# Kernel tuning notes

Hardware: AMD Instinct MI355X
Metric: run time of the kernel (lower is better)

Reference implementation:

```python
import jax, jax.numpy as jnp
import numpy as np

BN_EPS = 1e-5
NUM_HEADS = 16


def setup_inputs() -> dict:
    key = jax.random.key(0)
    k1, k2 = jax.random.split(key)
    B, F, E = 8, 1024, 1024
    x = jax.random.normal(k1, (B, F, E), dtype=jnp.float32)
    # xavier_uniform for Linear(E, 3E): bound = sqrt(6/(E + 3E))
    bound = float(np.sqrt(6.0 / (E + 3 * E)))
    W_qkv = jax.random.uniform(k2, (3 * E, E), minval=-bound, maxval=bound, dtype=jnp.float32)
    b_qkv = jnp.zeros((3 * E,), dtype=jnp.float32)
    gamma = jnp.ones((F,), dtype=jnp.float32)
    beta = jnp.zeros((F,), dtype=jnp.float32)
    return {"x": x, "gamma": gamma, "beta": beta, "W_qkv": W_qkv, "b_qkv": b_qkv}


def reference(x, gamma, beta, W_qkv, b_qkv):
    B, F, E = x.shape
    H = NUM_HEADS
    hd = E // H
    # BatchNorm1d(features_dim) in training mode: channels = F axis,
    # stats over (batch, embed) dims, biased variance.
    mean = jnp.mean(x, axis=(0, 2), keepdims=True)          # [1,F,1]
    var = jnp.mean((x - mean) ** 2, axis=(0, 2), keepdims=True)
    xn = (x - mean) * jax.lax.rsqrt(var + BN_EPS)
    xn = xn * gamma[None, :, None] + beta[None, :, None]
    # QKV projection: torch Linear -> xn @ W^T + b
    qkv = jnp.einsum('bfe,oe->bfo', xn, W_qkv) + b_qkv       # [B,F,3E]
    qkv = qkv.reshape(B, F, H, 3 * hd).transpose(0, 2, 1, 3) # [B,H,F,3hd]
    q, k, v = jnp.split(qkv, 3, axis=-1)                     # each [B,H,F,hd]
    scale = 1.0 / jnp.sqrt(jnp.float32(hd))
    logits = jnp.einsum('bhqd,bhkd->bhqk', q, k) * scale     # [B,H,F,F]
    attn = jax.nn.softmax(logits, axis=-1)
    values = jnp.einsum('bhqk,bhkd->bhqd', attn, v)          # [B,H,F,hd]
    values = values.transpose(0, 2, 1, 3).reshape(B, F, E)
    return values
```

## Files before the change

### kernel.cpp

```cpp
#include <hip/hip_runtime.h>

typedef unsigned short u16;
typedef unsigned int   u32;

typedef __bf16 bf16x8 __attribute__((ext_vector_type(8)));
typedef float  f32x4  __attribute__((ext_vector_type(4)));

typedef const __attribute__((address_space(1))) void* gas_ptr;
typedef __attribute__((address_space(3))) void* las_ptr;

__device__ __forceinline__ u16 f2bf(float f) {
  u32 u = __builtin_bit_cast(u32, f);
  u += 0x7fffu + ((u >> 16) & 1u);
  return (u16)(u >> 16);
}
__device__ __forceinline__ float bf2f(u16 u) {
  return __builtin_bit_cast(float, ((u32)u) << 16);
}
__device__ __forceinline__ u32 cvtpk(float a, float b) {
  u32 r;
  asm("v_cvt_pk_bf16_f32 %0, %1, %2" : "=v"(r) : "v"(a), "v"(b));
  return r;
}
__device__ __forceinline__ float fexp2(float x) {
  return __builtin_amdgcn_exp2f(x);
}

__global__ __launch_bounds__(256) void bn_norm_kernel(
    const float* __restrict__ x, const float* __restrict__ gamma,
    const float* __restrict__ beta, u16* __restrict__ xn) {
  const int F = 1024, E = 1024;
  int f = blockIdx.x;
  __shared__ float sh[8192];
  __shared__ float ps[4], pq[4], sc[2];

  const float* xf = x + (size_t)f * E;
  float ls = 0.f, lq = 0.f;
  for (int i = threadIdx.x; i < 8192; i += 256) {
    int b = i >> 10, e = i & 1023;
    float v = xf[(size_t)b * F * E + e];
    sh[i] = v;
    ls += v;
    lq += v * v;
  }
  #pragma unroll
  for (int o = 32; o > 0; o >>= 1) {
    ls += __shfl_down(ls, o, 64);
    lq += __shfl_down(lq, o, 64);
  }
  int w = threadIdx.x >> 6;
  if ((threadIdx.x & 63) == 0) { ps[w] = ls; pq[w] = lq; }
  __syncthreads();
  if (threadIdx.x == 0) {
    float s = ps[0] + ps[1] + ps[2] + ps[3];
    float q = pq[0] + pq[1] + pq[2] + pq[3];
    float mean = s * (1.f / 8192.f);
    float var = q * (1.f / 8192.f) - mean * mean;
    float scale = gamma[f] * rsqrtf(var + 1e-5f);
    sc[0] = scale;
    sc[1] = beta[f] - mean * scale;
  }
  __syncthreads();
  float scale = sc[0], shift = sc[1];
  for (int i = threadIdx.x; i < 8192; i += 256) {
    int b = i >> 10, e = i & 1023;
    xn[((size_t)(b * F + f)) * E + e] = f2bf(sh[i] * scale + shift);
  }
}

__global__ __launch_bounds__(256) void wconv_kernel(
    const float* __restrict__ W, u16* __restrict__ Wb) {
  const int total = 3072 * 1024 / 4;
  for (int i = blockIdx.x * 256 + threadIdx.x; i < total; i += gridDim.x * 256) {
    float4 v = ((const float4*)W)[i];
    ushort4 o;
    o.x = f2bf(v.x); o.y = f2bf(v.y); o.z = f2bf(v.z); o.w = f2bf(v.w);
    ((ushort4*)Wb)[i] = o;
  }
}

__global__ __launch_bounds__(512) void gemm_qkv_kernel(
    const u16* __restrict__ A, const u16* __restrict__ Bw,
    const float* __restrict__ bias, u16* __restrict__ C) {
  const int K = 1024, N = 3072;
  __shared__ u16 LA[2 * 16384];
  __shared__ u16 LB[2 * 16384];

  int bid = blockIdx.x;
  int m0 = (bid & 31) * 256, n0 = (bid >> 5) * 256;

  int tid = threadIdx.x;
  int lane = tid & 63, w = tid >> 6;
  int wm = w >> 2, wn = w & 3;
  int q = lane & 15, g = lane >> 4;
  int qs7 = q & 7;

  int srow8 = tid >> 3;
  int sc = tid & 7;

  f32x4 acc[8][4] = {};

  #define STAGE_A(buf, t)                                                    \
    do {                                                                     \
      _Pragma("unroll")                                                      \
      for (int j2 = 0; j2 < 4; ++j2) {                                       \
        int row = j2 * 64 + srow8;                                           \
        const u16* src = A + (size_t)(m0 + row) * K + (t) * 64               \
                           + ((sc ^ (row & 7)) * 8);                         \
        __builtin_amdgcn_global_load_lds((gas_ptr)src,                       \
            (las_ptr)&LA[(buf) * 16384 + row * 64 + sc * 8], 16, 0, 0);      \
      }                                                                      \
    } while (0)
  #define STAGE_B(buf, t)                                                    \
    do {                                                                     \
      _Pragma("unroll")                                                      \
      for (int j2 = 0; j2 < 4; ++j2) {                                       \
        int row = j2 * 64 + srow8;                                           \
        const u16* src = Bw + (size_t)(n0 + row) * K + (t) * 64              \
                            + ((sc ^ (row & 7)) * 8);                        \
        __builtin_amdgcn_global_load_lds((gas_ptr)src,                       \
            (las_ptr)&LB[(buf) * 16384 + row * 64 + sc * 8], 16, 0, 0);      \
      }                                                                      \
    } while (0)

  STAGE_A(0, 0);
  STAGE_B(0, 0);
  asm volatile("s_waitcnt vmcnt(0)" ::: "memory");
  __builtin_amdgcn_s_barrier();

  int aBase = (wm * 128 + q) * 64;
  int bBase = (wn * 64 + q) * 64;
  int c0 = (g ^ qs7) * 8;
  int c1 = ((4 + g) ^ qs7) * 8;

  for (int t = 0; t < 16; ++t) {
    int cur = t & 1, nxt = cur ^ 1;
    const u16* Ab = &LA[cur * 16384];
    const u16* Bb = &LB[cur * 16384];
    bool pf = t < 15;
    bf16x8 Br[4], Ar[4];

    #pragma unroll
    for (int ni = 0; ni < 4; ++ni)
      Br[ni] = __builtin_bit_cast(bf16x8, *(const int4*)&Bb[bBase + ni * 1024 + c0]);
    #pragma unroll
    for (int mi = 0; mi < 4; ++mi)
      Ar[mi] = __builtin_bit_cast(bf16x8, *(const int4*)&Ab[aBase + mi * 1024 + c0]);
    if (pf) STAGE_A(nxt, t + 1);
    __builtin_amdgcn_s_barrier();
    asm volatile("s_waitcnt lgkmcnt(0)" ::: "memory");
    __builtin_amdgcn_sched_barrier(0);
    __builtin_amdgcn_s_setprio(1);
    #pragma unroll
    for (int mi = 0; mi < 4; ++mi)
      #pragma unroll
      for (int ni = 0; ni < 4; ++ni)
        acc[mi][ni] = __builtin_amdgcn_mfma_f32_16x16x32_bf16(Ar[mi], Br[ni], acc[mi][ni], 0, 0, 0);
    __builtin_amdgcn_s_setprio(0);
    __builtin_amdgcn_s_barrier();

    #pragma unroll
    for (int mi = 0; mi < 4; ++mi)
      Ar[mi] = __builtin_bit_cast(bf16x8, *(const int4*)&Ab[aBase + (4 + mi) * 1024 + c0]);
    if (pf) STAGE_B(nxt, t + 1);
    __builtin_amdgcn_s_barrier();
    asm volatile("s_waitcnt lgkmcnt(0)" ::: "memory");
    __builtin_amdgcn_sched_barrier(0);
    __builtin_amdgcn_s_setprio(1);
    #pragma unroll
    for (int mi = 0; mi < 4; ++mi)
      #pragma unroll
      for (int ni = 0; ni < 4; ++ni)
        acc[4 + mi][ni] = __builtin_amdgcn_mfma_f32_16x16x32_bf16(Ar[mi], Br[ni], acc[4 + mi][ni], 0, 0, 0);
    __builtin_amdgcn_s_setprio(0);
    __builtin_amdgcn_s_barrier();

    #pragma unroll
    for (int ni = 0; ni < 4; ++ni)
      Br[ni] = __builtin_bit_cast(bf16x8, *(const int4*)&Bb[bBase + ni * 1024 + c1]);
    #pragma unroll
    for (int mi = 0; mi < 4; ++mi)
      Ar[mi] = __builtin_bit_cast(bf16x8, *(const int4*)&Ab[aBase + mi * 1024 + c1]);
    __builtin_amdgcn_s_barrier();
    asm volatile("s_waitcnt lgkmcnt(0)" ::: "memory");
    __builtin_amdgcn_sched_barrier(0);
    __builtin_amdgcn_s_setprio(1);
    #pragma unroll
    for (int mi = 0; mi < 4; ++mi)
      #pragma unroll
      for (int ni = 0; ni < 4; ++ni)
        acc[mi][ni] = __builtin_amdgcn_mfma_f32_16x16x32_bf16(Ar[mi], Br[ni], acc[mi][ni], 0, 0, 0);
    __builtin_amdgcn_s_setprio(0);
    __builtin_amdgcn_s_barrier();

    #pragma unroll
    for (int mi = 0; mi < 4; ++mi)
      Ar[mi] = __builtin_bit_cast(bf16x8, *(const int4*)&Ab[aBase + (4 + mi) * 1024 + c1]);
    __builtin_amdgcn_s_barrier();
    asm volatile("s_waitcnt lgkmcnt(0)" ::: "memory");
    __builtin_amdgcn_sched_barrier(0);
    __builtin_amdgcn_s_setprio(1);
    #pragma unroll
    for (int mi = 0; mi < 4; ++mi)
      #pragma unroll
      for (int ni = 0; ni < 4; ++ni)
        acc[4 + mi][ni] = __builtin_amdgcn_mfma_f32_16x16x32_bf16(Ar[mi], Br[ni], acc[4 + mi][ni], 0, 0, 0);
    __builtin_amdgcn_s_setprio(0);
    asm volatile("s_waitcnt vmcnt(0)" ::: "memory");
    __builtin_amdgcn_s_barrier();
  }
  #undef STAGE_A
  #undef STAGE_B

  #pragma unroll
  for (int ni = 0; ni < 4; ++ni) {
    int col = n0 + wn * 64 + ni * 16 + q;
    float bv = bias[col];
    #pragma unroll
    for (int mi = 0; mi < 8; ++mi) {
      int row = m0 + wm * 128 + mi * 16 + g * 4;
      #pragma unroll
      for (int j = 0; j < 4; ++j)
        C[(size_t)(row + j) * N + col] = f2bf(acc[mi][ni][j] + bv);
    }
  }
}

__global__ __launch_bounds__(256) void vt_kernel(
    const u16* __restrict__ qkv, u16* __restrict__ Vt) {
  __shared__ u16 T[64][72];
  int bh = blockIdx.y, b = bh >> 4, h = bh & 15;
  int f0 = blockIdx.x * 64;
  int t = threadIdx.x;
  int fl = t >> 2, c16 = (t & 3) * 16;
  const u16* src = qkv + (size_t)(b * 1024 + f0 + fl) * 3072 + h * 192 + 128 + c16;
  *(int4*)&T[fl][c16]     = *(const int4*)src;
  *(int4*)&T[fl][c16 + 8] = *(const int4*)(src + 8);
  __syncthreads();
  int dl = t >> 2, fc = (t & 3) * 16;
  u16 buf[16];
  #pragma unroll
  for (int j = 0; j < 16; ++j) {
    int c = fc + j;
    int m = c & 31;
    int a = ((m & 4) << 2) | ((m & 16) >> 1) | ((m & 8) >> 1) | (m & 3);
    buf[j] = T[(c & 32) | a][dl];
  }
  u16* dst = Vt + (size_t)bh * 65536 + (size_t)dl * 1024 + f0 + fc;
  *(int4*)dst       = *(int4*)&buf[0];
  *(int4*)(dst + 8) = *(int4*)&buf[8];
}

__global__ __launch_bounds__(256) void attn_kernel(
    const u16* __restrict__ qkv, const u16* __restrict__ Vt,
    float* __restrict__ out) {
  const int F = 1024, NQ = 3072;
  int bid = blockIdx.x;
  int xcd = bid & 7;
  int li  = bid >> 3;
  int bh  = ((li >> 4) << 3) | xcd;
  int ql  = li & 15;
  int w   = threadIdx.x >> 6;
  int lane = threadIdx.x & 63;
  int q = lane & 15, g = lane >> 4;
  int qs = q & 7;
  int q0 = ql * 64 + w * 16;
  int b = bh >> 4, h = bh & 15;

  const u16* base = qkv + (size_t)b * F * NQ + h * 192;
  const u16* VtBH = Vt + (size_t)bh * 65536;

  __shared__ u16 S[24576];

  int i8 = lane >> 3;
  int ic = lane & 7;

  const float qscale = 0.125f * 1.4426950408889634f;
  bf16x8 Qf0, Qf1;
  {
    const u16* qp = base + (size_t)(q0 + q) * NQ + g * 8;
    union { int4 v; u16 u[8]; } uu0, uu1;
    uu0.v = *(const int4*)(qp);
    uu1.v = *(const int4*)(qp + 32);
    union { u32 w4[4]; bf16x8 v; } p0, p1;
    #pragma unroll
    for (int j = 0; j < 4; ++j) {
      p0.w4[j] = cvtpk(bf2f(uu0.u[2 * j]) * qscale, bf2f(uu0.u[2 * j + 1]) * qscale);
      p1.w4[j] = cvtpk(bf2f(uu1.u[2 * j]) * qscale, bf2f(uu1.u[2 * j + 1]) * qscale);
    }
    Qf0 = p0.v; Qf1 = p1.v;
  }

  f32x4 acc[4] = {};
  float m = 0.0f, lsum = 0.f;

  #define STAGE(buf, kt)                                                       \
    do {                                                                       \
      int kb_ = (kt) * 64;                                                     \
      _Pragma("unroll")                                                        \
      for (int rr = 0; rr < 2; ++rr) {                                         \
        int r_ = rr * 32 + w * 8 + i8;                                         \
        int sc_ = (ic ^ (r_ & 7)) * 8;                                         \
        const u16* ks_ = base + (size_t)(kb_ + r_) * NQ + 64 + sc_;            \
        const u16* vs_ = VtBH + (size_t)r_ * 1024 + kb_ + sc_;                 \
        __builtin_amdgcn_global_load_lds((gas_ptr)ks_,                         \
            (las_ptr)&S[(buf) * 4096 + (rr * 32 + w * 8) * 64], 16, 0, 0);     \
        __builtin_amdgcn_global_load_lds((gas_ptr)vs_,                         \
            (las_ptr)&S[12288 + (buf) * 4096 + (rr * 32 + w * 8) * 64], 16, 0, 0);\
      }                                                                        \
    } while (0)

  __builtin_amdgcn_sched_barrier(0);
  STAGE(0, 0);
  STAGE(1, 1);
  asm volatile("s_waitcnt vmcnt(4)" ::: "memory");
  __builtin_amdgcn_s_barrier();
  __builtin_amdgcn_sched_barrier(0);

  #pragma unroll
  for (int kt = 0; kt < 16; ++kt) {
    const int cur = kt % 3;
    const int stg = (kt + 2) % 3;
    if (kt < 14) STAGE(stg, kt + 2);

    const u16* Kb = &S[cur * 4096];
    const u16* Vb = &S[12288 + cur * 4096];

    f32x4 s[4];
    f32x4 seed = {-m, -m, -m, -m};
    __builtin_amdgcn_s_setprio(1);
    #pragma unroll
    for (int ks = 0; ks < 4; ++ks) {
      int row = ks * 16 + q;
      int4 k0 = *(const int4*)&Kb[row * 64 + ((g ^ qs) * 8)];
      int4 k1 = *(const int4*)&Kb[row * 64 + (((4 + g) ^ qs) * 8)];
      f32x4 sv = seed;
      sv = __builtin_amdgcn_mfma_f32_16x16x32_bf16(__builtin_bit_cast(bf16x8, k0), Qf0, sv, 0, 0, 0);
      sv = __builtin_amdgcn_mfma_f32_16x16x32_bf16(__builtin_bit_cast(bf16x8, k1), Qf1, sv, 0, 0, 0);
      s[ks] = sv;
    }
    __builtin_amdgcn_s_setprio(0);

    float a0 = fmaxf(fmaxf(s[0][0], s[0][1]), s[0][2]);
    float a1 = fmaxf(fmaxf(s[0][3], s[1][0]), s[1][1]);
    float a2 = fmaxf(fmaxf(s[1][2], s[1][3]), s[2][0]);
    float a3 = fmaxf(fmaxf(s[2][1], s[2][2]), s[2][3]);
    float a4 = fmaxf(fmaxf(s[3][0], s[3][1]), s[3][2]);
    float tmx = fmaxf(fmaxf(fmaxf(a0, a1), a2), fmaxf(fmaxf(a3, a4), s[3][3]));

    float p[16];
    if (__builtin_expect(__any(tmx > 8.0f), 0)) {
      float tr = fmaxf(tmx, __shfl_xor(tmx, 16, 64));
      tr = fmaxf(tr, __shfl_xor(tr, 32, 64));
      float dm = fmaxf(tr, 0.f);
      float alpha = fexp2(-dm);
      lsum *= alpha;
      acc[0] *= alpha; acc[1] *= alpha; acc[2] *= alpha; acc[3] *= alpha;
      m += dm;
      #pragma unroll
      for (int ks = 0; ks < 4; ++ks) {
        p[ks * 4 + 0] = fexp2(s[ks][0] - dm);
        p[ks * 4 + 1] = fexp2(s[ks][1] - dm);
        p[ks * 4 + 2] = fexp2(s[ks][2] - dm);
        p[ks * 4 + 3] = fexp2(s[ks][3] - dm);
      }
    } else {
      #pragma unroll
      for (int ks = 0; ks < 4; ++ks) {
        p[ks * 4 + 0] = fexp2(s[ks][0]);
        p[ks * 4 + 1] = fexp2(s[ks][1]);
        p[ks * 4 + 2] = fexp2(s[ks][2]);
        p[ks * 4 + 3] = fexp2(s[ks][3]);
      }
    }
    float q01 = p[0] + p[1],   q23 = p[2] + p[3];
    float q45 = p[4] + p[5],   q67 = p[6] + p[7];
    float q89 = p[8] + p[9],   qab = p[10] + p[11];
    float qcd = p[12] + p[13], qef = p[14] + p[15];
    lsum += ((q01 + q23) + (q45 + q67)) + ((q89 + qab) + (qcd + qef));

    union { u32 w4[4]; bf16x8 v; } pb0, pb1;
    pb0.w4[0] = cvtpk(p[0], p[1]);   pb0.w4[1] = cvtpk(p[2], p[3]);
    pb0.w4[2] = cvtpk(p[4], p[5]);   pb0.w4[3] = cvtpk(p[6], p[7]);
    pb1.w4[0] = cvtpk(p[8], p[9]);   pb1.w4[1] = cvtpk(p[10], p[11]);
    pb1.w4[2] = cvtpk(p[12], p[13]); pb1.w4[3] = cvtpk(p[14], p[15]);

    __builtin_amdgcn_s_setprio(1);
    #pragma unroll
    for (int dt = 0; dt < 4; ++dt) {
      int row = dt * 16 + q;
      int4 v0 = *(const int4*)&Vb[row * 64 + ((g ^ qs) * 8)];
      int4 v1 = *(const int4*)&Vb[row * 64 + (((4 + g) ^ qs) * 8)];
      acc[dt] = __builtin_amdgcn_mfma_f32_16x16x32_bf16(__builtin_bit_cast(bf16x8, v0), pb0.v, acc[dt], 0, 0, 0);
      acc[dt] = __builtin_amdgcn_mfma_f32_16x16x32_bf16(__builtin_bit_cast(bf16x8, v1), pb1.v, acc[dt], 0, 0, 0);
    }
    __builtin_amdgcn_s_setprio(0);

    if (kt < 14) {
      asm volatile("s_waitcnt vmcnt(4)" ::: "memory");
    } else {
      asm volatile("s_waitcnt vmcnt(0)" ::: "memory");
    }
    __builtin_amdgcn_s_barrier();
    __builtin_amdgcn_sched_barrier(0);
  }
  #undef STAGE

  lsum += __shfl_xor(lsum, 16, 64);
  lsum += __shfl_xor(lsum, 32, 64);
  float inv = 1.0f / lsum;

  float* oT = (float*)S + (size_t)w * 1088;
  #pragma unroll
  for (int dt = 0; dt < 4; ++dt) {
    oT[(dt * 16 + g * 4 + 0) * 17 + q] = acc[dt][0] * inv;
    oT[(dt * 16 + g * 4 + 1) * 17 + q] = acc[dt][1] * inv;
    oT[(dt * 16 + g * 4 + 2) * 17 + q] = acc[dt][2] * inv;
    oT[(dt * 16 + g * 4 + 3) * 17 + q] = acc[dt][3] * inv;
  }
  asm volatile("s_waitcnt lgkmcnt(0)" ::: "memory");
  int oq = lane >> 2, dc = (lane & 3) * 16;
  float* orow = out + (size_t)(b * F + q0 + oq) * 1024 + h * 64 + dc;
  #pragma unroll
  for (int c4 = 0; c4 < 4; ++c4) {
    float4 v;
    v.x = oT[(dc + c4 * 4 + 0) * 17 + oq];
    v.y = oT[(dc + c4 * 4 + 1) * 17 + oq];
    v.z = oT[(dc + c4 * 4 + 2) * 17 + oq];
    v.w = oT[(dc + c4 * 4 + 3) * 17 + oq];
    *(float4*)(orow + c4 * 4) = v;
  }
}

extern "C" void kernel_launch(void* const* d_in, const int* in_sizes, int n_in,
                              void* d_out, int out_size, void* d_ws, size_t ws_size,
                              hipStream_t stream) {
  const float* x     = (const float*)d_in[0];
  const float* gamma = (const float*)d_in[1];
  const float* beta  = (const float*)d_in[2];
  const float* W     = (const float*)d_in[3];
  const float* bias  = (const float*)d_in[4];
  float* out = (float*)d_out;

  char* ws = (char*)d_ws;
  u16* xn  = (u16*)ws;
  u16* Wb  = (u16*)(ws + (size_t)16 * 1024 * 1024);
  u16* qkv = (u16*)(ws + (size_t)22 * 1024 * 1024);
  u16* Vt  = (u16*)(ws + (size_t)70 * 1024 * 1024);

  bn_norm_kernel<<<1024, 256, 0, stream>>>(x, gamma, beta, xn);
  wconv_kernel<<<768, 256, 0, stream>>>(W, Wb);
  gemm_qkv_kernel<<<384, 512, 0, stream>>>(xn, Wb, bias, qkv);
  vt_kernel<<<dim3(16, 128), 256, 0, stream>>>(qkv, Vt);
  attn_kernel<<<2048, 256, 0, stream>>>(qkv, Vt, out);
}
```

Measured before the change: 170.6 us.

## Split K-tiles into half-tile LDS slots for deeper GEMM prefetch pipeline

Restructures the QKV GEMM's shared-memory staging so each 64-wide K tile is held as two 32-wide halves. Loads are issued 1.5 tiles ahead, and partial vmcnt waits replace the full drain at each iteration end. It also swaps the row XOR swizzle for a new pattern suited to 32-column rows and remaps block IDs so neighbouring blocks share tiles in cache. The goal is to hide global-load latency behind the MFMAs, at the cost of more delicate wait-count bookkeeping.

```diff
diff --git a/kernel.cpp b/kernel.cpp
--- a/kernel.cpp
+++ b/kernel.cpp
@@ -83,70 +83,67 @@
     const u16* __restrict__ A, const u16* __restrict__ Bw,
     const float* __restrict__ bias, u16* __restrict__ C) {
   const int K = 1024, N = 3072;
-  __shared__ u16 LA[2 * 16384];
-  __shared__ u16 LB[2 * 16384];
-
-  int bid = blockIdx.x;
-  int m0 = (bid & 31) * 256, n0 = (bid >> 5) * 256;
+  __shared__ u16 LS[65536];
+
+  int li = (blockIdx.x & 7) * 48 + (blockIdx.x >> 3);
+  int m0 = (li & 31) * 256, n0 = (li >> 5) * 256;
 
   int tid = threadIdx.x;
   int lane = tid & 63, w = tid >> 6;
   int wm = w >> 2, wn = w & 3;
   int q = lane & 15, g = lane >> 4;
-  int qs7 = q & 7;
-
-  int srow8 = tid >> 3;
-  int sc = tid & 7;
+  int qh = (q >> 1) & 3;
+  int cfr = (g ^ qh) * 8;
 
   f32x4 acc[8][4] = {};
 
-  #define STAGE_A(buf, t)                                                    \
-    do {                                                                     \
-      _Pragma("unroll")                                                      \
-      for (int j2 = 0; j2 < 4; ++j2) {                                       \
-        int row = j2 * 64 + srow8;                                           \
-        const u16* src = A + (size_t)(m0 + row) * K + (t) * 64               \
-                           + ((sc ^ (row & 7)) * 8);                         \
-        __builtin_amdgcn_global_load_lds((gas_ptr)src,                       \
-            (las_ptr)&LA[(buf) * 16384 + row * 64 + sc * 8], 16, 0, 0);      \
-      }                                                                      \
+  #define STAGE_A(slot, h, t)                                                  \
+    do {                                                                       \
+      _Pragma("unroll")                                                        \
+      for (int j = 0; j < 2; ++j) {                                            \
+        int row = j * 128 + (tid >> 2);                                        \
+        int cc = (tid & 3) ^ ((row >> 1) & 3);                                 \
+        const u16* src = A + (size_t)(m0 + row) * K + (t) * 64 + (h) * 32 + cc * 8; \
+        __builtin_amdgcn_global_load_lds((gas_ptr)src,                         \
+            (las_ptr)&LS[(slot) * 16384 + (h) * 8192 + j * 4096 + tid * 8], 16, 0, 0); \
+      }                                                                        \
     } while (0)
-  #define STAGE_B(buf, t)                                                    \
-    do {                                                                     \
-      _Pragma("unroll")                                                      \
-      for (int j2 = 0; j2 < 4; ++j2) {                                       \
-        int row = j2 * 64 + srow8;                                           \
-        const u16* src = Bw + (size_t)(n0 + row) * K + (t) * 64              \
-                            + ((sc ^ (row & 7)) * 8);                        \
-        __builtin_amdgcn_global_load_lds((gas_ptr)src,                       \
-            (las_ptr)&LB[(buf) * 16384 + row * 64 + sc * 8], 16, 0, 0);      \
-      }                                                                      \
+  #define STAGE_B(slot, h, t)                                                  \
+    do {                                                                       \
+      _Pragma("unroll")                                                        \
+      for (int j = 0; j < 2; ++j) {                                            \
+        int row = j * 128 + (tid >> 2);                                        \
+        int cc = (tid & 3) ^ ((row >> 1) & 3);                                 \
+        const u16* src = Bw + (size_t)(n0 + row) * K + (t) * 64 + (h) * 32 + cc * 8; \
+        __builtin_amdgcn_global_load_lds((gas_ptr)src,                         \
+            (las_ptr)&LS[32768 + (slot) * 16384 + (h) * 8192 + j * 4096 + tid * 8], 16, 0, 0); \
+      }                                                                        \
     } while (0)
 
-  STAGE_A(0, 0);
-  STAGE_B(0, 0);
-  asm volatile("s_waitcnt vmcnt(0)" ::: "memory");
+  STAGE_A(0, 0, 0); STAGE_B(0, 0, 0);
+  STAGE_A(0, 1, 0); STAGE_B(0, 1, 0);
+  STAGE_A(1, 0, 1); STAGE_B(1, 0, 1);
+  asm volatile("s_waitcnt vmcnt(8)" ::: "memory");
   __builtin_amdgcn_s_barrier();
 
-  int aBase = (wm * 128 + q) * 64;
-  int bBase = (wn * 64 + q) * 64;
-  int c0 = (g ^ qs7) * 8;
-  int c1 = ((4 + g) ^ qs7) * 8;
-
-  for (int t = 0; t < 16; ++t) {
-    int cur = t & 1, nxt = cur ^ 1;
-    const u16* Ab = &LA[cur * 16384];
-    const u16* Bb = &LB[cur * 16384];
-    bool pf = t < 15;
-    bf16x8 Br[4], Ar[4];
+  for (int kt = 0; kt < 16; ++kt) {
+    int d = kt & 1, dn = (kt + 1) & 1;
+    const u16* Ab0 = &LS[d * 16384];
+    const u16* Bb0 = &LS[32768 + d * 16384];
+    const u16* Ab1 = Ab0 + 8192;
+    const u16* Bb1 = Bb0 + 8192;
+    int aOff = (wm * 128 + q) * 32 + cfr;
+    int bOff = (wn * 64 + q) * 32 + cfr;
+
+    bf16x8 Ar[4], Br[4];
 
     #pragma unroll
     for (int ni = 0; ni < 4; ++ni)
-      Br[ni] = __builtin_bit_cast(bf16x8, *(const int4*)&Bb[bBase + ni * 1024 + c0]);
-    #pragma unroll
-    for (int mi = 0; mi < 4; ++mi)
-      Ar[mi] = __builtin_bit_cast(bf16x8, *(const int4*)&Ab[aBase + mi * 1024 + c0]);
-    if (pf) STAGE_A(nxt, t + 1);
+      Br[ni] = __builtin_bit_cast(bf16x8, *(const int4*)&Bb0[bOff + ni * 512]);
+    #pragma unroll
+    for (int mi = 0; mi < 4; ++mi)
+      Ar[mi] = __builtin_bit_cast(bf16x8, *(const int4*)&Ab0[aOff + mi * 512]);
+    if (kt < 15) STAGE_A(dn, 1, kt + 1);
     __builtin_amdgcn_s_barrier();
     asm volatile("s_waitcnt lgkmcnt(0)" ::: "memory");
     __builtin_amdgcn_sched_barrier(0);
@@ -161,8 +158,8 @@
 
     #pragma unroll
     for (int mi = 0; mi < 4; ++mi)
-      Ar[mi] = __builtin_bit_cast(bf16x8, *(const int4*)&Ab[aBase + (4 + mi) * 1024 + c0]);
-    if (pf) STAGE_B(nxt, t + 1);
+      Ar[mi] = __builtin_bit_cast(bf16x8, *(const int4*)&Ab0[aOff + (4 + mi) * 512]);
+    if (kt < 15) STAGE_B(dn, 1, kt + 1);
     __builtin_amdgcn_s_barrier();
     asm volatile("s_waitcnt lgkmcnt(0)" ::: "memory");
     __builtin_amdgcn_sched_barrier(0);
@@ -173,14 +170,17 @@
       for (int ni = 0; ni < 4; ++ni)
         acc[4 + mi][ni] = __builtin_amdgcn_mfma_f32_16x16x32_bf16(Ar[mi], Br[ni], acc[4 + mi][ni], 0, 0, 0);
     __builtin_amdgcn_s_setprio(0);
+    if (kt < 15) { asm volatile("s_waitcnt vmcnt(8)" ::: "memory"); }
+    else         { asm volatile("s_waitcnt vmcnt(0)" ::: "memory"); }
     __builtin_amdgcn_s_barrier();
 
     #pragma unroll
     for (int ni = 0; ni < 4; ++ni)
-      Br[ni] = __builtin_bit_cast(bf16x8, *(const int4*)&Bb[bBase + ni * 1024 + c1]);
-    #pragma unroll
-    for (int mi = 0; mi < 4; ++mi)
-      Ar[mi] = __builtin_bit_cast(bf16x8, *(const int4*)&Ab[aBase + mi * 1024 + c1]);
+      Br[ni] = __builtin_bit_cast(bf16x8, *(const int4*)&Bb1[bOff + ni * 512]);
+    #pragma unroll
+    for (int mi = 0; mi < 4; ++mi)
+      Ar[mi] = __builtin_bit_cast(bf16x8, *(const int4*)&Ab1[aOff + mi * 512]);
+    if (kt < 14) STAGE_A(d, 0, kt + 2);
     __builtin_amdgcn_s_barrier();
     asm volatile("s_waitcnt lgkmcnt(0)" ::: "memory");
     __builtin_amdgcn_sched_barrier(0);
@@ -195,7 +195,8 @@
 
     #pragma unroll
     for (int mi = 0; mi < 4; ++mi)
-      Ar[mi] = __builtin_bit_cast(bf16x8, *(const int4*)&Ab[aBase + (4 + mi) * 1024 + c1]);
+      Ar[mi] = __builtin_bit_cast(bf16x8, *(const int4*)&Ab1[aOff + (4 + mi) * 512]);
+    if (kt < 14) STAGE_B(d, 0, kt + 2);
     __builtin_amdgcn_s_barrier();
     asm volatile("s_waitcnt lgkmcnt(0)" ::: "memory");
     __builtin_amdgcn_sched_barrier(0);
@@ -206,7 +207,9 @@
       for (int ni = 0; ni < 4; ++ni)
         acc[4 + mi][ni] = __builtin_amdgcn_mfma_f32_16x16x32_bf16(Ar[mi], Br[ni], acc[4 + mi][ni], 0, 0, 0);
     __builtin_amdgcn_s_setprio(0);
-    asm volatile("s_waitcnt vmcnt(0)" ::: "memory");
+    if (kt < 14)      { asm volatile("s_waitcnt vmcnt(8)" ::: "memory"); }
+    else if (kt == 14){ asm volatile("s_waitcnt vmcnt(4)" ::: "memory"); }
+    else              { asm volatile("s_waitcnt vmcnt(0)" ::: "memory"); }
     __builtin_amdgcn_s_barrier();
   }
   #undef STAGE_A
```

Result: faster. 164.1 us (-3.8%).
